# Performance work log

Measured on AMD Instinct MI355X. Metric: run time of the kernel, lower is better.

The kernel has to match this reference:

```python
import jax, jax.numpy as jnp
import numpy as np

REG_MAX = 16
NUM_CLASSES = 80
STRIDES = (8, 16, 32)
FEAT_SIZES = ((80, 80), (40, 40), (20, 20))
CLS_DIM = 256
REG_DIM = 256
B = 16


def setup_inputs() -> dict:
    key = jax.random.key(0)
    ks = jax.random.split(key, 32)
    inp = {}
    i = 0
    for l, (H, W) in enumerate(FEAT_SIZES):
        inp[f"cls_feat{l}"] = jax.random.normal(ks[i], (B, CLS_DIM, H, W), jnp.float32); i += 1
        inp[f"reg_feat{l}"] = jax.random.normal(ks[i], (B, REG_DIM, H, W), jnp.float32); i += 1
    bias_init = -float(np.log((1.0 - 0.01) / 0.01))
    for l in range(3):
        inp[f"obj_w{l}"] = jax.random.normal(ks[i], (1, REG_DIM), jnp.float32) * 0.02; i += 1
        inp[f"obj_b{l}"] = jnp.full((1,), bias_init, jnp.float32)
        inp[f"cls_w{l}"] = jax.random.normal(ks[i], (NUM_CLASSES, CLS_DIM), jnp.float32) * 0.02; i += 1
        inp[f"cls_b{l}"] = jnp.full((NUM_CLASSES,), bias_init, jnp.float32)
        inp[f"reg_w{l}"] = jax.random.normal(ks[i], (4 * REG_MAX, REG_DIM), jnp.float32) * 0.02; i += 1
        inp[f"reg_b{l}"] = jnp.ones((4 * REG_MAX,), jnp.float32)
    return inp


def _anchors(H, W, stride):
    ay, ax = jnp.meshgrid(jnp.arange(H, dtype=jnp.float32), jnp.arange(W, dtype=jnp.float32), indexing="ij")
    a = jnp.stack([ax, ay], axis=-1).reshape(-1, 2)  # [HW, 2] (x, y)
    return (a + 0.5) * stride


def _level(cls_feat, reg_feat, obj_w, obj_b, cls_w, cls_b, reg_w, reg_b, stride):
    Bb, _, H, W = cls_feat.shape
    M = H * W
    # 1x1 convs as channel contractions; output in [B, H, W, O] then flatten to [B, M, O]
    obj = (jnp.einsum("bchw,oc->bhwo", reg_feat, obj_w) + obj_b).reshape(Bb, M, 1)
    cls = (jnp.einsum("bchw,oc->bhwo", cls_feat, cls_w) + cls_b).reshape(Bb, M, NUM_CLASSES)
    reg = (jnp.einsum("bchw,oc->bhwo", reg_feat, reg_w) + reg_b).reshape(Bb, M, 4 * REG_MAX)
    # DFL decode: softmax over bins, expectation with proj = linspace(0, reg_max, reg_max)
    proj = jnp.linspace(0.0, float(REG_MAX), REG_MAX)
    dist = jax.nn.softmax(reg.reshape(Bb, M, 4, REG_MAX), axis=-1)
    reg_d = jnp.einsum("bmfr,r->bmf", dist, proj)  # [B, M, 4] (l, t, r, b)
    anchors = _anchors(H, W, stride)  # [M, 2]
    x1y1 = anchors[None] - reg_d[..., :2] * stride
    x2y2 = anchors[None] + reg_d[..., 2:] * stride
    box = jnp.concatenate([x1y1, x2y2], axis=-1)  # [B, M, 4]
    return jnp.concatenate([obj, cls, reg, box], axis=-1)  # [B, M, 1+80+64+4]


def reference(cls_feat0, cls_feat1, cls_feat2, reg_feat0, reg_feat1, reg_feat2,
              obj_w0, obj_b0, cls_w0, cls_b0, reg_w0, reg_b0,
              obj_w1, obj_b1, cls_w1, cls_b1, reg_w1, reg_b1,
              obj_w2, obj_b2, cls_w2, cls_b2, reg_w2, reg_b2):
    lvl0 = _level(cls_feat0, reg_feat0, obj_w0, obj_b0, cls_w0, cls_b0, reg_w0, reg_b0, STRIDES[0])
    lvl1 = _level(cls_feat1, reg_feat1, obj_w1, obj_b1, cls_w1, cls_b1, reg_w1, reg_b1, STRIDES[1])
    lvl2 = _level(cls_feat2, reg_feat2, obj_w2, obj_b2, cls_w2, cls_b2, reg_w2, reg_b2, STRIDES[2])
    # concat anchors along M: [B, 8400, 149]
    return jnp.concatenate([lvl0, lvl1, lvl2], axis=1)
```

## Files before the change

### kernel.cpp

```cpp
#include <hip/hip_runtime.h>
#include <stdint.h>

typedef __attribute__((ext_vector_type(4))) float f32x4;
typedef __attribute__((ext_vector_type(8))) short s16x8;
typedef float f32x4u __attribute__((ext_vector_type(4), aligned(4)));
typedef unsigned short u16x4 __attribute__((ext_vector_type(4)));

struct Params {
  const float* cls_feat[3];
  const float* reg_feat[3];
  const float* obj_w[3];
  const float* obj_b[3];
  const float* cls_w[3];
  const float* cls_b[3];
  const float* reg_w[3];
  const float* reg_b[3];
  unsigned short* wbf;
  float* out;
};

__device__ __forceinline__ unsigned short f2bf(float f) {
  unsigned int u = __builtin_bit_cast(unsigned int, f);
  u = (u + 0x7FFFu + ((u >> 16) & 1u)) >> 16;
  return (unsigned short)u;
}

__global__ __launch_bounds__(64) void prep_weights(Params p) {
  const int R = blockIdx.x;
  const int kind  = R / 240;
  const int rem   = R - kind * 240;
  const int level = rem / 80;
  const int o     = rem - level * 80;
  const float* src = nullptr;
  if (kind == 0)      src = p.cls_w[level] + (size_t)o * 256;
  else if (o < 64)    src = p.reg_w[level] + (size_t)o * 256;
  else if (o == 64)   src = p.obj_w[level];
  unsigned short* dst = p.wbf + (size_t)R * 256 + threadIdx.x * 4;
  u16x4 h = {0, 0, 0, 0};
  if (src) {
    f32x4 f = *(const f32x4u*)(src + threadIdx.x * 4);
    h[0] = f2bf(f[0]); h[1] = f2bf(f[1]); h[2] = f2bf(f[2]); h[3] = f2bf(f[3]);
  }
  *(u16x4*)dst = h;
}

__global__ __launch_bounds__(256) void head_kernel(Params p) {
  const int tid  = threadIdx.x;
  const int lane = tid & 63;
  const int wave = tid >> 6;
  const int quad = lane >> 4;
  const int col  = lane & 15;
  const int kind = blockIdx.y;

  const int t = blockIdx.x * 4 + wave;
  const int b = t / 525;
  const int r = t - b * 525;
  int level, m0;
  if (r < 400)      { level = 0; m0 = r * 16; }
  else if (r < 500) { level = 1; m0 = (r - 400) * 16; }
  else              { level = 2; m0 = (r - 500) * 16; }

  const int   LM_[3]   = {6400, 1600, 400};
  const int   LW_[3]   = {80, 40, 20};
  const float LS_[3]   = {8.f, 16.f, 32.f};
  const int   LOFF_[3] = {0, 6400, 8000};
  const int   Mlvl = LM_[level];
  const float strd = LS_[level];

  const float* feat = (kind ? p.reg_feat[level] : p.cls_feat[level])
                      + (size_t)b * 256 * (size_t)Mlvl + m0 + col;
  s16x8 bfrag[8];
  #pragma unroll
  for (int s = 0; s < 8; ++s) {
    float f[8];
    #pragma unroll
    for (int j = 0; j < 8; ++j)
      f[j] = feat[(size_t)(s * 32 + quad * 8 + j) * Mlvl];
    s16x8 h;
    #pragma unroll
    for (int j = 0; j < 8; ++j) h[j] = (short)f2bf(f[j]);
    bfrag[s] = h;
  }

  const unsigned short* wbase = p.wbf + (size_t)((kind * 3 + level) * 80) * 256;
  const size_t outbase = (size_t)b * 8400 + LOFF_[level] + m0;
  float* out = p.out;
  const size_t rowoff = (outbase + col) * 149;

  float g[4];

  #pragma unroll
  for (int tile = 0; tile < 5; ++tile) {
    const unsigned short* wp = wbase + (size_t)(tile * 16 + col) * 256 + quad * 8;
    f32x4 d = {0.f, 0.f, 0.f, 0.f};
    #pragma unroll
    for (int s = 0; s < 8; ++s) {
      s16x8 a = *(const s16x8*)(wp + s * 32);
      d = __builtin_amdgcn_mfma_f32_16x16x32_bf16(a, bfrag[s], d, 0, 0, 0);
    }

    if (kind == 0) {
      f32x4 bias = *(const f32x4u*)(p.cls_b[level] + tile * 16 + quad * 4);
      f32x4 v = d + bias;
      *(f32x4u*)(out + rowoff + 1 + tile * 16 + quad * 4) = v;
    } else if (tile < 4) {
      f32x4 bias = *(const f32x4u*)(p.reg_b[level] + tile * 16 + quad * 4);
      f32x4 v = d + bias;
      *(f32x4u*)(out + rowoff + 81 + tile * 16 + quad * 4) = v;
      float mx = fmaxf(fmaxf(v[0], v[1]), fmaxf(v[2], v[3]));
      mx = fmaxf(mx, __shfl_xor(mx, 16, 64));
      mx = fmaxf(mx, __shfl_xor(mx, 32, 64));
      const float e0 = __expf(v[0] - mx), e1 = __expf(v[1] - mx);
      const float e2 = __expf(v[2] - mx), e3 = __expf(v[3] - mx);
      float s = e0 + e1 + e2 + e3;
      const float q4 = (float)(quad * 4);
      float n = q4 * e0 + (q4 + 1.f) * e1 + (q4 + 2.f) * e2 + (q4 + 3.f) * e3;
      s += __shfl_xor(s, 16, 64); s += __shfl_xor(s, 32, 64);
      n += __shfl_xor(n, 16, 64); n += __shfl_xor(n, 32, 64);
      g[tile] = (16.f / 15.f) * n / s;
    } else {
      if (quad == 0) out[rowoff] = d[0] + p.obj_b[level][0];
    }
  }

  if (kind == 1 && quad == 1) {
    const int mg = m0 + col;
    const int hh = mg / LW_[level];
    const int ww = mg - hh * LW_[level];
    const float ax = (ww + 0.5f) * strd;
    const float ay = (hh + 0.5f) * strd;
    f32x4 box;
    box[0] = ax - g[0] * strd;
    box[1] = ay - g[1] * strd;
    box[2] = ax + g[2] * strd;
    box[3] = ay + g[3] * strd;
    *(f32x4u*)(out + rowoff + 145) = box;
  }
}

extern "C" void kernel_launch(void* const* d_in, const int* in_sizes, int n_in,
                              void* d_out, int out_size, void* d_ws, size_t ws_size,
                              hipStream_t stream) {
  (void)in_sizes; (void)n_in; (void)out_size; (void)ws_size;
  Params p;
  p.cls_feat[0] = (const float*)d_in[0];
  p.reg_feat[0] = (const float*)d_in[1];
  p.cls_feat[1] = (const float*)d_in[2];
  p.reg_feat[1] = (const float*)d_in[3];
  p.cls_feat[2] = (const float*)d_in[4];
  p.reg_feat[2] = (const float*)d_in[5];
  for (int l = 0; l < 3; ++l) {
    const int base = 6 + l * 6;
    p.obj_w[l] = (const float*)d_in[base + 0];
    p.obj_b[l] = (const float*)d_in[base + 1];
    p.cls_w[l] = (const float*)d_in[base + 2];
    p.cls_b[l] = (const float*)d_in[base + 3];
    p.reg_w[l] = (const float*)d_in[base + 4];
    p.reg_b[l] = (const float*)d_in[base + 5];
  }
  p.wbf = (unsigned short*)d_ws;
  p.out = (float*)d_out;

  hipLaunchKernelGGL(prep_weights, dim3(480), dim3(64), 0, stream, p);
  hipLaunchKernelGGL(head_kernel, dim3(2100, 2), dim3(256), 0, stream, p);
}
```

Measured before the change: 397.8 us.

## Stage output rows in shared memory for coalesced stores, merging cls and reg waves

Each block now handles 64 anchors for both the cls and reg branches using 8 waves, and writes results into a padded shared-memory tile instead of scattering strided 149-float rows directly to global memory. After a barrier, the tile is written out as one contiguous, coalesced span. This replaces many unaligned partial-row stores with full-line writes, at the cost of about 40KB of LDS per block and an extra barrier. Feature loads are also batched four slices at a time to expose more memory parallelism.

```diff
diff --git a/kernel.cpp b/kernel.cpp
--- a/kernel.cpp
+++ b/kernel.cpp
@@ -44,49 +44,61 @@
   *(u16x4*)dst = h;
 }
 
-__global__ __launch_bounds__(256) void head_kernel(Params p) {
+#define SP 156
+
+__global__ __launch_bounds__(512, 4) void head_kernel(Params p) {
   const int tid  = threadIdx.x;
   const int lane = tid & 63;
   const int wave = tid >> 6;
   const int quad = lane >> 4;
   const int col  = lane & 15;
-  const int kind = blockIdx.y;
+  const int kind = wave >> 2;
+  const int msub = wave & 3;
 
-  const int t = blockIdx.x * 4 + wave;
-  const int b = t / 525;
-  const int r = t - b * 525;
-  int level, m0;
-  if (r < 400)      { level = 0; m0 = r * 16; }
-  else if (r < 500) { level = 1; m0 = (r - 400) * 16; }
-  else              { level = 2; m0 = (r - 500) * 16; }
+  const int bx = blockIdx.x;
+  const int b  = bx / 132;
+  const int t  = bx - b * 132;
+  int level, tloc;
+  if (t < 100)      { level = 0; tloc = t; }
+  else if (t < 125) { level = 1; tloc = t - 100; }
+  else              { level = 2; tloc = t - 125; }
 
-  const int   LM_[3]   = {6400, 1600, 400};
-  const int   LW_[3]   = {80, 40, 20};
-  const float LS_[3]   = {8.f, 16.f, 32.f};
-  const int   LOFF_[3] = {0, 6400, 8000};
-  const int   Mlvl = LM_[level];
-  const float strd = LS_[level];
+  const int   Mlvl = (level == 0) ? 6400 : (level == 1) ? 1600 : 400;
+  const int   Moff = (level == 0) ? 0    : (level == 1) ? 6400 : 8000;
+  const float strd = (level == 0) ? 8.f  : (level == 1) ? 16.f : 32.f;
 
-  const float* feat = (kind ? p.reg_feat[level] : p.cls_feat[level])
-                      + (size_t)b * 256 * (size_t)Mlvl + m0 + col;
+  const int m0t = tloc * 64;
+  const int m0  = m0t + msub * 16;
+  int valid = Mlvl - m0t; if (valid > 64) valid = 64;
+
+  __shared__ float sout[64 * SP];
+
+  const float* featb = (kind ? p.reg_feat[level] : p.cls_feat[level])
+                       + (size_t)b * 256 * (size_t)Mlvl;
+  int mg = m0 + col; if (mg > Mlvl - 1) mg = Mlvl - 1;
+  const float* fp = featb + mg + (size_t)(quad * 8) * Mlvl;
+
   s16x8 bfrag[8];
   #pragma unroll
-  for (int s = 0; s < 8; ++s) {
-    float f[8];
+  for (int half = 0; half < 2; ++half) {
+    float f[4][8];
     #pragma unroll
-    for (int j = 0; j < 8; ++j)
-      f[j] = feat[(size_t)(s * 32 + quad * 8 + j) * Mlvl];
-    s16x8 h;
+    for (int s = 0; s < 4; ++s) {
+      #pragma unroll
+      for (int j = 0; j < 8; ++j)
+        f[s][j] = fp[(size_t)((half * 4 + s) * 32 + j) * Mlvl];
+    }
     #pragma unroll
-    for (int j = 0; j < 8; ++j) h[j] = (short)f2bf(f[j]);
-    bfrag[s] = h;
+    for (int s = 0; s < 4; ++s) {
+      s16x8 h;
+      #pragma unroll
+      for (int j = 0; j < 8; ++j) h[j] = (short)f2bf(f[s][j]);
+      bfrag[half * 4 + s] = h;
+    }
   }
 
   const unsigned short* wbase = p.wbf + (size_t)((kind * 3 + level) * 80) * 256;
-  const size_t outbase = (size_t)b * 8400 + LOFF_[level] + m0;
-  float* out = p.out;
-  const size_t rowoff = (outbase + col) * 149;
-
+  float* srow = &sout[(msub * 16 + col) * SP];
   float g[4];
 
   #pragma unroll
@@ -101,40 +113,51 @@
 
     if (kind == 0) {
       f32x4 bias = *(const f32x4u*)(p.cls_b[level] + tile * 16 + quad * 4);
-      f32x4 v = d + bias;
-      *(f32x4u*)(out + rowoff + 1 + tile * 16 + quad * 4) = v;
+      *(f32x4*)(srow + 4 + tile * 16 + quad * 4) = d + bias;
     } else if (tile < 4) {
       f32x4 bias = *(const f32x4u*)(p.reg_b[level] + tile * 16 + quad * 4);
       f32x4 v = d + bias;
-      *(f32x4u*)(out + rowoff + 81 + tile * 16 + quad * 4) = v;
+      *(f32x4*)(srow + 84 + tile * 16 + quad * 4) = v;
       float mx = fmaxf(fmaxf(v[0], v[1]), fmaxf(v[2], v[3]));
       mx = fmaxf(mx, __shfl_xor(mx, 16, 64));
       mx = fmaxf(mx, __shfl_xor(mx, 32, 64));
       const float e0 = __expf(v[0] - mx), e1 = __expf(v[1] - mx);
       const float e2 = __expf(v[2] - mx), e3 = __expf(v[3] - mx);
-      float s = e0 + e1 + e2 + e3;
+      float sden = e0 + e1 + e2 + e3;
       const float q4 = (float)(quad * 4);
-      float n = q4 * e0 + (q4 + 1.f) * e1 + (q4 + 2.f) * e2 + (q4 + 3.f) * e3;
-      s += __shfl_xor(s, 16, 64); s += __shfl_xor(s, 32, 64);
-      n += __shfl_xor(n, 16, 64); n += __shfl_xor(n, 32, 64);
-      g[tile] = (16.f / 15.f) * n / s;
+      float num = q4 * e0 + (q4 + 1.f) * e1 + (q4 + 2.f) * e2 + (q4 + 3.f) * e3;
+      sden += __shfl_xor(sden, 16, 64); sden += __shfl_xor(sden, 32, 64);
+      num  += __shfl_xor(num, 16, 64);  num  += __shfl_xor(num, 32, 64);
+      g[tile] = (16.f / 15.f) * num / sden;
     } else {
-      if (quad == 0) out[rowoff] = d[0] + p.obj_b[level][0];
+      if (quad == 0) srow[3] = d[0] + p.obj_b[level][0];
     }
   }
 
-  if (kind == 1 && quad == 1) {
-    const int mg = m0 + col;
-    const int hh = mg / LW_[level];
-    const int ww = mg - hh * LW_[level];
+  if (kind == 1) {
+    const int LW = (level == 0) ? 80 : (level == 1) ? 40 : 20;
+    const int hh = (level == 0) ? mg / 80 : (level == 1) ? mg / 40 : mg / 20;
+    const int ww = mg - hh * LW;
     const float ax = (ww + 0.5f) * strd;
     const float ay = (hh + 0.5f) * strd;
-    f32x4 box;
-    box[0] = ax - g[0] * strd;
-    box[1] = ay - g[1] * strd;
-    box[2] = ax + g[2] * strd;
-    box[3] = ay + g[3] * strd;
-    *(f32x4u*)(out + rowoff + 145) = box;
+    if (quad == 1) {
+      f32x4 box;
+      box[0] = ax - g[0] * strd;
+      box[1] = ay - g[1] * strd;
+      box[2] = ax + g[2] * strd;
+      box[3] = ay + g[3] * strd;
+      *(f32x4*)(srow + 148) = box;
+    }
+  }
+
+  __syncthreads();
+
+  float* outp = p.out + ((size_t)b * 8400 + Moff + m0t) * 149;
+  const int ndw = valid * 149;
+  for (int i = tid; i < ndw; i += 512) {
+    const int m = i / 149;
+    const int c = i - m * 149;
+    outp[i] = sout[m * SP + c + 3];
   }
 }
 
@@ -162,5 +185,5 @@
   p.out = (float*)d_out;
 
   hipLaunchKernelGGL(prep_weights, dim3(480), dim3(64), 0, stream, p);
-  hipLaunchKernelGGL(head_kernel, dim3(2100, 2), dim3(256), 0, stream, p);
+  hipLaunchKernelGGL(head_kernel, dim3(16 * 132), dim3(512), 0, stream, p);
 }
```

New measurement: 385.0 us. -3.2%, faster.
